# Performance work log

Measured on AMD Instinct MI355X. Metric: run time of the kernel, lower is better.

## Reference

```python
import jax, jax.numpy as jnp
import numpy as np

VOLRADIUS = 256.0  # init kwarg
NSTEPS = 64        # raymarch steps; dt chosen so NSTEPS*dt covers the box segment


def setup_inputs() -> dict:
    key = jax.random.key(0)
    ks = jax.random.split(key, 6)
    B, H, W, K, S = 1, 128, 128, 64, 16
    # camera ~2 box-radii in front of the volume (raw/world units, divided by VOLRADIUS in forward)
    viewpos = jnp.array([[0.0, 0.0, -2.0 * VOLRADIUS]], dtype=jnp.float32)
    viewpos = viewpos + 0.01 * VOLRADIUS * jax.random.normal(ks[0], (B, 3), dtype=jnp.float32)
    viewrot = jnp.tile(jnp.eye(3, dtype=jnp.float32)[None], (B, 1, 1))
    # pinhole rays looking at the box (tan(half-fov)=0.6 so the [-1,1]^3 box fills the frame)
    v, u = jnp.meshgrid(jnp.linspace(-1.0, 1.0, H), jnp.linspace(-1.0, 1.0, W), indexing='ij')
    d = jnp.stack([u * 0.6, v * 0.6, jnp.ones_like(u)], axis=-1)
    raydir = (d / jnp.linalg.norm(d, axis=-1, keepdims=True)).astype(jnp.float32)
    raydir = jnp.tile(raydir[None], (B, 1, 1, 1))
    # volumetric primitive payload + placement (normalized [-1,1] volume coords)
    template = jax.random.uniform(ks[1], (B, K, 4, S, S, S), dtype=jnp.float32)
    primpos = jax.random.uniform(ks[2], (B, K, 3), dtype=jnp.float32, minval=-0.7, maxval=0.7)
    q, _ = jnp.linalg.qr(jax.random.normal(ks[3], (B, K, 3, 3), dtype=jnp.float32))
    primrot = q.astype(jnp.float32)
    primscale = jax.random.uniform(ks[4], (B, K, 3), dtype=jnp.float32, minval=4.0, maxval=8.0)
    # raw dt (world units); forward divides by VOLRADIUS -> normalized step 2.2/NSTEPS
    dt = jnp.float32(2.2 / NSTEPS * VOLRADIUS)
    return dict(viewpos=viewpos, viewrot=viewrot, raydir=raydir, template=template,
                primpos=primpos, primrot=primrot, primscale=primscale, dt=dt)


def _sample_primitives(template, pos, primpos, primrot, primscale):
    """Sum of trilinearly-sampled RGBA over all primitives containing each point.
    template: [B,K,4,S,S,S], pos: [B,H,W,3] -> [B,H,W,4]"""
    B, K = template.shape[0], template.shape[1]
    S = template.shape[-1]
    xm = pos[:, :, :, None, :] - primpos[:, None, None, :, :]              # [B,H,W,K,3]
    # local coords: R^T (x - p) scaled by primscale (inverse half-extent)
    y = jnp.einsum('bhwki,bkij->bhwkj', xm, primrot) * primscale[:, None, None]
    inside = jnp.all(jnp.abs(y) < 1.0, axis=-1)                             # [B,H,W,K]
    g = (y + 1.0) * (0.5 * (S - 1))                                         # align_corners voxel coords
    g0 = jnp.clip(jnp.floor(g), 0.0, S - 2).astype(jnp.int32)
    f = g - g0.astype(g.dtype)
    x0, y0, z0 = g0[..., 0], g0[..., 1], g0[..., 2]                        # x->W, y->H, z->D
    fx, fy, fz = f[..., 0, None], f[..., 1, None], f[..., 2, None]
    tpl = jnp.moveaxis(template, 2, -1)                                     # [B,K,S,S,S,4]
    bidx = jnp.arange(B)[:, None, None, None]
    kidx = jnp.arange(K)[None, None, None, :]
    def gat(zi, yi, xi):
        return tpl[bidx, kidx, zi, yi, xi]                                  # [B,H,W,K,4]
    c00 = gat(z0, y0, x0) * (1 - fx) + gat(z0, y0, x0 + 1) * fx
    c01 = gat(z0, y0 + 1, x0) * (1 - fx) + gat(z0, y0 + 1, x0 + 1) * fx
    c10 = gat(z0 + 1, y0, x0) * (1 - fx) + gat(z0 + 1, y0, x0 + 1) * fx
    c11 = gat(z0 + 1, y0 + 1, x0) * (1 - fx) + gat(z0 + 1, y0 + 1, x0 + 1) * fx
    c = (c00 * (1 - fy) + c01 * fy) * (1 - fz) + (c10 * (1 - fy) + c11 * fy) * fz
    return jnp.einsum('bhwk,bhwkc->bhwc', inside.astype(c.dtype), c)        # [B,H,W,4]


def reference(viewpos, viewrot, raydir, template, primpos, primrot, primscale, dt):
    vp = viewpos / VOLRADIUS
    dtn = dt / VOLRADIUS
    # ray - AABB slab intersection with the [-1,1]^3 volume (no_grad in original)
    t1 = (-1.0 - vp[:, None, None, :]) / raydir
    t2 = (1.0 - vp[:, None, None, :]) / raydir
    tmin = jnp.maximum(jnp.minimum(t1[..., 0], t2[..., 0]),
                       jnp.maximum(jnp.minimum(t1[..., 1], t2[..., 1]),
                                   jnp.minimum(t1[..., 2], t2[..., 2])))
    tmax = jnp.minimum(jnp.maximum(t1[..., 0], t2[..., 0]),
                       jnp.minimum(jnp.maximum(t1[..., 1], t2[..., 1]),
                                   jnp.maximum(t1[..., 2], t2[..., 2])))
    inter = tmin < tmax
    tmin_ = jax.lax.stop_gradient(jnp.where(inter, tmin, 0.0))
    tmax_ = jax.lax.stop_gradient(jnp.where(inter, tmax, 0.0))
    t0 = jnp.maximum(tmin_, 0.0)
    rayposbeg = vp[:, None, None, :] + raydir * tmin_[..., None]
    rayposend = vp[:, None, None, :] + raydir * tmax_[..., None]

    def step(rgba, i):
        t = t0 + i.astype(t0.dtype) * dtn                                   # [B,H,W]
        valid = (t < tmax_).astype(rgba.dtype)
        pos = vp[:, None, None, :] + raydir * t[..., None]
        s = _sample_primitives(template, pos, primpos, primrot, primscale)  # [B,H,W,4]
        alpha = s[..., 3] * dtn * valid
        # saturating additive compositing (mvpraymarch): contrib = min(a+da,1)-a
        contrib = jnp.minimum(rgba[..., 3] + alpha, 1.0) - rgba[..., 3]
        rgba = rgba + jnp.concatenate([s[..., :3], jnp.ones_like(s[..., :1])], -1) * contrib[..., None]
        return rgba, None

    rgba0 = jnp.zeros(raydir.shape[:3] + (4,), raydir.dtype)
    rgba, _ = jax.lax.scan(step, rgba0, jnp.arange(NSTEPS))
    return (jnp.transpose(rgba, (0, 3, 1, 2)), rayposbeg, rayposend)
```

## Files before the change

### kernel.cpp

```cpp
#include <hip/hip_runtime.h>

#define HH 128
#define WW 128
#define KK 64
#define SS 16
#define S3 (SS * SS * SS)
#define VOLRADIUS 256.0f
#define CULL_EPS 1e-3f

template <int CTRL, int RM>
__device__ __forceinline__ float dpp_add(float x) {
    int y = __builtin_amdgcn_update_dpp(0, __float_as_int(x), CTRL, RM, 0xF, false);
    return x + __int_as_float(y);
}
__device__ __forceinline__ float wave_incl_scan(float x) {
    x = dpp_add<0x111, 0xF>(x);
    x = dpp_add<0x112, 0xF>(x);
    x = dpp_add<0x114, 0xF>(x);
    x = dpp_add<0x118, 0xF>(x);
    x = dpp_add<0x142, 0xA>(x);
    x = dpp_add<0x143, 0xC>(x);
    return x;
}

#define LERP4(a, b, f) make_float4(a.x*(1.f-(f)) + b.x*(f), a.y*(1.f-(f)) + b.y*(f), \
                                   a.z*(1.f-(f)) + b.z*(f), a.w*(1.f-(f)) + b.w*(f))

__global__ __launch_bounds__(256) void transpose_tpl(const float* __restrict__ tpl,
                                                     float4* __restrict__ tw) {
    int i = blockIdx.x * blockDim.x + threadIdx.x;
    if (i >= KK * S3) return;
    int k = i >> 12, v = i & (S3 - 1);
    const float* src = tpl + ((size_t)k * 4 * S3) + v;
    tw[i] = make_float4(src[0], src[S3], src[2 * S3], src[3 * S3]);
}

template <bool TR>
__global__ __launch_bounds__(256, 6) void raymarch_kernel(
    const float* __restrict__ viewpos,
    const float* __restrict__ raydir,
    const float* __restrict__ tpl,
    const float* __restrict__ primpos,
    const float* __restrict__ primrot,
    const float* __restrict__ primscale,
    const float* __restrict__ dtp,
    const float4* __restrict__ tw,
    float* __restrict__ out)
{
    const int lane = threadIdx.x & 63;
    const int pix  = (int)((blockIdx.x * blockDim.x + threadIdx.x) >> 6);
    if (pix >= HH * WW) return;

    const float vx = viewpos[0] / VOLRADIUS;
    const float vy = viewpos[1] / VOLRADIUS;
    const float vz = viewpos[2] / VOLRADIUS;
    const float dtn = dtp[0] / VOLRADIUS;

    const float Rx = raydir[pix*3+0], Ry = raydir[pix*3+1], Rz = raydir[pix*3+2];

    float t1x = (-1.f-vx)/Rx, t2x = (1.f-vx)/Rx;
    float t1y = (-1.f-vy)/Ry, t2y = (1.f-vy)/Ry;
    float t1z = (-1.f-vz)/Rz, t2z = (1.f-vz)/Rz;
    float tmin = fmaxf(fminf(t1x,t2x), fmaxf(fminf(t1y,t2y), fminf(t1z,t2z)));
    float tmax = fminf(fmaxf(t1x,t2x), fminf(fmaxf(t1y,t2y), fmaxf(t1z,t2z)));
    bool inter = tmin < tmax;
    float tmin_ = inter ? tmin : 0.f;
    float tmax_ = inter ? tmax : 0.f;
    float t0 = fmaxf(tmin_, 0.f);
    float t = t0 + (float)lane * dtn;
    const bool tvalid = t < tmax_;
    const float posx = vx + Rx*t;
    const float posy = vy + Ry*t;
    const float posz = vz + Rz*t;

    unsigned long long mask;
    {
        const float px = primpos[lane*3+0], py = primpos[lane*3+1], pz = primpos[lane*3+2];
        const float r00 = primrot[lane*9+0], r01 = primrot[lane*9+1], r02 = primrot[lane*9+2];
        const float r10 = primrot[lane*9+3], r11 = primrot[lane*9+4], r12 = primrot[lane*9+5];
        const float r20 = primrot[lane*9+6], r21 = primrot[lane*9+7], r22 = primrot[lane*9+8];
        const float sx = primscale[lane*3+0], sy = primscale[lane*3+1], sz = primscale[lane*3+2];
        float bb[3], dd[3];
        bb[0] = ((vx-px)*r00 + (vy-py)*r10 + (vz-pz)*r20) * sx;
        bb[1] = ((vx-px)*r01 + (vy-py)*r11 + (vz-pz)*r21) * sy;
        bb[2] = ((vx-px)*r02 + (vy-py)*r12 + (vz-pz)*r22) * sz;
        dd[0] = (Rx*r00 + Ry*r10 + Rz*r20) * sx;
        dd[1] = (Rx*r01 + Ry*r11 + Rz*r21) * sy;
        dd[2] = (Rx*r02 + Ry*r12 + Rz*r22) * sz;
        float tend = fminf(tmax_, t0 + 63.f*dtn);
        float te = t0, tx = tend;
#pragma unroll
        for (int j = 0; j < 3; ++j) {
            float ta, tb2;
            if (fabsf(dd[j]) > 1e-12f) {
                float inv = 1.f / dd[j];
                ta  = (-1.f - CULL_EPS - bb[j]) * inv;
                tb2 = ( 1.f + CULL_EPS - bb[j]) * inv;
            } else {
                bool ok = fabsf(bb[j]) <= 1.f + CULL_EPS;
                ta  = ok ? -3e38f :  3e38f;
                tb2 = ok ?  3e38f : -3e38f;
            }
            te = fmaxf(te, fminf(ta, tb2));
            tx = fminf(tx, fmaxf(ta, tb2));
        }
        mask = __ballot(te <= tx);
    }

    float sv0 = 0.f, sv1 = 0.f, sv2 = 0.f, sv3 = 0.f;

    while (mask) {
        const int ku = __builtin_amdgcn_readfirstlane(__ffsll(mask) - 1);
        mask &= mask - 1;
        const float qpx = primpos[ku*3+0], qpy = primpos[ku*3+1], qpz = primpos[ku*3+2];
        const float q00 = primrot[ku*9+0], q01 = primrot[ku*9+1], q02 = primrot[ku*9+2];
        const float q10 = primrot[ku*9+3], q11 = primrot[ku*9+4], q12 = primrot[ku*9+5];
        const float q20 = primrot[ku*9+6], q21 = primrot[ku*9+7], q22 = primrot[ku*9+8];
        const float qsx = primscale[ku*3+0], qsy = primscale[ku*3+1], qsz = primscale[ku*3+2];

        float xmx = posx-qpx, xmy = posy-qpy, xmz = posz-qpz;
        float y0 = (xmx*q00 + xmy*q10 + xmz*q20) * qsx;
        float y1 = (xmx*q01 + xmy*q11 + xmz*q21) * qsy;
        float y2 = (xmx*q02 + xmy*q12 + xmz*q22) * qsz;
        bool samp = tvalid && fabsf(y0) < 1.f && fabsf(y1) < 1.f && fabsf(y2) < 1.f;

        if (samp) {
            float gx = (y0+1.f)*(0.5f*(SS-1));
            float gy = (y1+1.f)*(0.5f*(SS-1));
            float gz = (y2+1.f)*(0.5f*(SS-1));
            int x0  = min(max((int)floorf(gx), 0), SS-2);
            int y0i = min(max((int)floorf(gy), 0), SS-2);
            int z0  = min(max((int)floorf(gz), 0), SS-2);
            float fx = gx-(float)x0, fy = gy-(float)y0i, fz = gz-(float)z0;
            int idx = z0*(SS*SS) + y0i*SS + x0;

            if (TR) {
                const float4* tb = tw + ((size_t)ku << 12) + idx;
                float4 c000 = tb[0],          c001 = tb[1];
                float4 c010 = tb[SS],         c011 = tb[SS+1];
                float4 c100 = tb[SS*SS],      c101 = tb[SS*SS+1];
                float4 c110 = tb[SS*SS+SS],   c111 = tb[SS*SS+SS+1];
                float4 c00 = LERP4(c000, c001, fx);
                float4 c01 = LERP4(c010, c011, fx);
                float4 c10 = LERP4(c100, c101, fx);
                float4 c11 = LERP4(c110, c111, fx);
                float4 e0  = LERP4(c00, c01, fy);
                float4 e1  = LERP4(c10, c11, fy);
                sv0 += e0.x*(1.f-fz) + e1.x*fz;
                sv1 += e0.y*(1.f-fz) + e1.y*fz;
                sv2 += e0.z*(1.f-fz) + e1.z*fz;
                sv3 += e0.w*(1.f-fz) + e1.w*fz;
            } else {
                const float* tp = tpl + (size_t)ku * (4 * S3);
                float sv[4];
#pragma unroll
                for (int c = 0; c < 4; ++c) {
                    const float* tc = tp + c * S3;
                    float c000 = tc[idx],              c001 = tc[idx+1];
                    float c010 = tc[idx+SS],           c011 = tc[idx+SS+1];
                    float c100 = tc[idx+SS*SS],        c101 = tc[idx+SS*SS+1];
                    float c110 = tc[idx+SS*SS+SS],     c111 = tc[idx+SS*SS+SS+1];
                    float c00 = c000*(1.f-fx) + c001*fx;
                    float c01 = c010*(1.f-fx) + c011*fx;
                    float c10 = c100*(1.f-fx) + c101*fx;
                    float c11 = c110*(1.f-fx) + c111*fx;
                    sv[c] = (c00*(1.f-fy) + c01*fy)*(1.f-fz)
                          + (c10*(1.f-fy) + c11*fy)*fz;
                }
                sv0 += sv[0]; sv1 += sv[1]; sv2 += sv[2]; sv3 += sv[3];
            }
        }
    }

    float alpha = tvalid ? sv3 * dtn : 0.f;
    float A = wave_incl_scan(alpha);
    float Aex = __shfl_up(A, 1, 64);
    if (lane == 0) Aex = 0.f;
    float contrib = fminf(Aex + alpha, 1.f) - fminf(Aex, 1.f);
    float cr = wave_incl_scan(sv0 * contrib);
    float cg = wave_incl_scan(sv1 * contrib);
    float cb = wave_incl_scan(sv2 * contrib);
    float At = fminf(A, 1.f);

    if (lane == 63) {
        out[0*HH*WW + pix] = cr;
        out[1*HH*WW + pix] = cg;
        out[2*HH*WW + pix] = cb;
        out[3*HH*WW + pix] = At;
        const int b1 = 4*HH*WW;
        out[b1 + pix*3+0] = vx + Rx*tmin_;
        out[b1 + pix*3+1] = vy + Ry*tmin_;
        out[b1 + pix*3+2] = vz + Rz*tmin_;
        const int b2 = b1 + HH*WW*3;
        out[b2 + pix*3+0] = vx + Rx*tmax_;
        out[b2 + pix*3+1] = vy + Ry*tmax_;
        out[b2 + pix*3+2] = vz + Rz*tmax_;
    }
}

extern "C" void kernel_launch(void* const* d_in, const int* in_sizes, int n_in,
                              void* d_out, int out_size, void* d_ws, size_t ws_size,
                              hipStream_t stream) {
    const float* viewpos   = (const float*)d_in[0];
    const float* raydir    = (const float*)d_in[2];
    const float* tpl       = (const float*)d_in[3];
    const float* primpos   = (const float*)d_in[4];
    const float* primrot   = (const float*)d_in[5];
    const float* primscale = (const float*)d_in[6];
    const float* dtp       = (const float*)d_in[7];
    float* out = (float*)d_out;

    const size_t twbytes = (size_t)KK * S3 * 4 * sizeof(float);
    dim3 block(256), grid(HH * WW * 64 / 256);

    if (ws_size >= twbytes) {
        transpose_tpl<<<dim3((KK * S3 + 255) / 256), block, 0, stream>>>(tpl, (float4*)d_ws);
        raymarch_kernel<true><<<grid, block, 0, stream>>>(
            viewpos, raydir, tpl, primpos, primrot, primscale, dtp,
            (const float4*)d_ws, out);
    } else {
        raymarch_kernel<false><<<grid, block, 0, stream>>>(
            viewpos, raydir, tpl, primpos, primrot, primscale, dtp,
            (const float4*)d_ws, out);
    }
}
```

Before: 36.06 us.

## Software-pipeline primitive gathers in two stages and remap wave-to-pixel order

The transposed-template path now issues the eight float4 gathers for the next culled primitive before interpolating the current one. This double-buffers loads across iterations to hide global memory latency. Out-of-box samples load index 0 with zero weight instead of branching. Launch bounds drop to 4 waves per EU to make room for the extra registers, and the wave-to-pixel mapping is permuted (pix = (wid&63)<<8 | wid>>6), which changes which rays share a block and how they hit the cache.

```diff
diff --git a/kernel.cpp b/kernel.cpp
--- a/kernel.cpp
+++ b/kernel.cpp
@@ -35,8 +35,55 @@
     tw[i] = make_float4(src[0], src[S3], src[2 * S3], src[3 * S3]);
 }
 
+#define DECL_STAGE(S) \
+    float4 c0##S, c1##S, c2##S, c3##S, c4##S, c5##S, c6##S, c7##S; \
+    float fx##S, fy##S, fz##S, w##S;
+
+#define STAGE_ISSUE(S) { \
+    const int ku = __builtin_amdgcn_readfirstlane(__ffsll(mask) - 1); \
+    mask &= mask - 1; \
+    const float qpx = primpos[ku*3+0], qpy = primpos[ku*3+1], qpz = primpos[ku*3+2]; \
+    const float q00 = primrot[ku*9+0], q01 = primrot[ku*9+1], q02 = primrot[ku*9+2]; \
+    const float q10 = primrot[ku*9+3], q11 = primrot[ku*9+4], q12 = primrot[ku*9+5]; \
+    const float q20 = primrot[ku*9+6], q21 = primrot[ku*9+7], q22 = primrot[ku*9+8]; \
+    const float qsx = primscale[ku*3+0], qsy = primscale[ku*3+1], qsz = primscale[ku*3+2]; \
+    float xmx = posx-qpx, xmy = posy-qpy, xmz = posz-qpz; \
+    float y0 = (xmx*q00 + xmy*q10 + xmz*q20) * qsx; \
+    float y1 = (xmx*q01 + xmy*q11 + xmz*q21) * qsy; \
+    float y2 = (xmx*q02 + xmy*q12 + xmz*q22) * qsz; \
+    bool samp = tvalid && fabsf(y0) < 1.f && fabsf(y1) < 1.f && fabsf(y2) < 1.f; \
+    float gx = (y0+1.f)*(0.5f*(SS-1)); \
+    float gy = (y1+1.f)*(0.5f*(SS-1)); \
+    float gz = (y2+1.f)*(0.5f*(SS-1)); \
+    int x0  = min(max((int)floorf(gx), 0), SS-2); \
+    int y0i = min(max((int)floorf(gy), 0), SS-2); \
+    int z0  = min(max((int)floorf(gz), 0), SS-2); \
+    fx##S = gx-(float)x0; fy##S = gy-(float)y0i; fz##S = gz-(float)z0; \
+    w##S  = samp ? 1.f : 0.f; \
+    int idx = samp ? (z0*(SS*SS) + y0i*SS + x0) : 0; \
+    const float4* tb = tw + ((size_t)ku << 12) + idx; \
+    c0##S = tb[0];          c1##S = tb[1]; \
+    c2##S = tb[SS];         c3##S = tb[SS+1]; \
+    c4##S = tb[SS*SS];      c5##S = tb[SS*SS+1]; \
+    c6##S = tb[SS*SS+SS];   c7##S = tb[SS*SS+SS+1]; \
+}
+
+#define STAGE_CONSUME(S) { \
+    float4 c00 = LERP4(c0##S, c1##S, fx##S); \
+    float4 c01 = LERP4(c2##S, c3##S, fx##S); \
+    float4 c10 = LERP4(c4##S, c5##S, fx##S); \
+    float4 c11 = LERP4(c6##S, c7##S, fx##S); \
+    float4 e0  = LERP4(c00, c01, fy##S); \
+    float4 e1  = LERP4(c10, c11, fy##S); \
+    float fzv = fz##S, wv = w##S; \
+    sv0 += (e0.x*(1.f-fzv) + e1.x*fzv) * wv; \
+    sv1 += (e0.y*(1.f-fzv) + e1.y*fzv) * wv; \
+    sv2 += (e0.z*(1.f-fzv) + e1.z*fzv) * wv; \
+    sv3 += (e0.w*(1.f-fzv) + e1.w*fzv) * wv; \
+}
+
 template <bool TR>
-__global__ __launch_bounds__(256, 6) void raymarch_kernel(
+__global__ __launch_bounds__(256, 4) void raymarch_kernel(
     const float* __restrict__ viewpos,
     const float* __restrict__ raydir,
     const float* __restrict__ tpl,
@@ -48,8 +95,9 @@
     float* __restrict__ out)
 {
     const int lane = threadIdx.x & 63;
-    const int pix  = (int)((blockIdx.x * blockDim.x + threadIdx.x) >> 6);
-    if (pix >= HH * WW) return;
+    const int wid  = (int)((blockIdx.x * blockDim.x + threadIdx.x) >> 6);
+    if (wid >= HH * WW) return;
+    const int pix = ((wid & 63) << 8) | (wid >> 6);
 
     const float vx = viewpos[0] / VOLRADIUS;
     const float vy = viewpos[1] / VOLRADIUS;
@@ -109,48 +157,45 @@
 
     float sv0 = 0.f, sv1 = 0.f, sv2 = 0.f, sv3 = 0.f;
 
-    while (mask) {
-        const int ku = __builtin_amdgcn_readfirstlane(__ffsll(mask) - 1);
-        mask &= mask - 1;
-        const float qpx = primpos[ku*3+0], qpy = primpos[ku*3+1], qpz = primpos[ku*3+2];
-        const float q00 = primrot[ku*9+0], q01 = primrot[ku*9+1], q02 = primrot[ku*9+2];
-        const float q10 = primrot[ku*9+3], q11 = primrot[ku*9+4], q12 = primrot[ku*9+5];
-        const float q20 = primrot[ku*9+6], q21 = primrot[ku*9+7], q22 = primrot[ku*9+8];
-        const float qsx = primscale[ku*3+0], qsy = primscale[ku*3+1], qsz = primscale[ku*3+2];
-
-        float xmx = posx-qpx, xmy = posy-qpy, xmz = posz-qpz;
-        float y0 = (xmx*q00 + xmy*q10 + xmz*q20) * qsx;
-        float y1 = (xmx*q01 + xmy*q11 + xmz*q21) * qsy;
-        float y2 = (xmx*q02 + xmy*q12 + xmz*q22) * qsz;
-        bool samp = tvalid && fabsf(y0) < 1.f && fabsf(y1) < 1.f && fabsf(y2) < 1.f;
-
-        if (samp) {
-            float gx = (y0+1.f)*(0.5f*(SS-1));
-            float gy = (y1+1.f)*(0.5f*(SS-1));
-            float gz = (y2+1.f)*(0.5f*(SS-1));
-            int x0  = min(max((int)floorf(gx), 0), SS-2);
-            int y0i = min(max((int)floorf(gy), 0), SS-2);
-            int z0  = min(max((int)floorf(gz), 0), SS-2);
-            float fx = gx-(float)x0, fy = gy-(float)y0i, fz = gz-(float)z0;
-            int idx = z0*(SS*SS) + y0i*SS + x0;
-
-            if (TR) {
-                const float4* tb = tw + ((size_t)ku << 12) + idx;
-                float4 c000 = tb[0],          c001 = tb[1];
-                float4 c010 = tb[SS],         c011 = tb[SS+1];
-                float4 c100 = tb[SS*SS],      c101 = tb[SS*SS+1];
-                float4 c110 = tb[SS*SS+SS],   c111 = tb[SS*SS+SS+1];
-                float4 c00 = LERP4(c000, c001, fx);
-                float4 c01 = LERP4(c010, c011, fx);
-                float4 c10 = LERP4(c100, c101, fx);
-                float4 c11 = LERP4(c110, c111, fx);
-                float4 e0  = LERP4(c00, c01, fy);
-                float4 e1  = LERP4(c10, c11, fy);
-                sv0 += e0.x*(1.f-fz) + e1.x*fz;
-                sv1 += e0.y*(1.f-fz) + e1.y*fz;
-                sv2 += e0.z*(1.f-fz) + e1.z*fz;
-                sv3 += e0.w*(1.f-fz) + e1.w*fz;
-            } else {
+    if (TR) {
+        DECL_STAGE(A)
+        DECL_STAGE(B)
+        if (mask) {
+            STAGE_ISSUE(A)
+            for (;;) {
+                bool haveB = (mask != 0ull);
+                if (haveB) STAGE_ISSUE(B)
+                STAGE_CONSUME(A)
+                if (!haveB) break;
+                bool haveA = (mask != 0ull);
+                if (haveA) STAGE_ISSUE(A)
+                STAGE_CONSUME(B)
+                if (!haveA) break;
+            }
+        }
+    } else {
+        while (mask) {
+            const int ku = __builtin_amdgcn_readfirstlane(__ffsll(mask) - 1);
+            mask &= mask - 1;
+            const float qpx = primpos[ku*3+0], qpy = primpos[ku*3+1], qpz = primpos[ku*3+2];
+            const float q00 = primrot[ku*9+0], q01 = primrot[ku*9+1], q02 = primrot[ku*9+2];
+            const float q10 = primrot[ku*9+3], q11 = primrot[ku*9+4], q12 = primrot[ku*9+5];
+            const float q20 = primrot[ku*9+6], q21 = primrot[ku*9+7], q22 = primrot[ku*9+8];
+            const float qsx = primscale[ku*3+0], qsy = primscale[ku*3+1], qsz = primscale[ku*3+2];
+            float xmx = posx-qpx, xmy = posy-qpy, xmz = posz-qpz;
+            float y0 = (xmx*q00 + xmy*q10 + xmz*q20) * qsx;
+            float y1 = (xmx*q01 + xmy*q11 + xmz*q21) * qsy;
+            float y2 = (xmx*q02 + xmy*q12 + xmz*q22) * qsz;
+            bool samp = tvalid && fabsf(y0) < 1.f && fabsf(y1) < 1.f && fabsf(y2) < 1.f;
+            if (samp) {
+                float gx = (y0+1.f)*(0.5f*(SS-1));
+                float gy = (y1+1.f)*(0.5f*(SS-1));
+                float gz = (y2+1.f)*(0.5f*(SS-1));
+                int x0  = min(max((int)floorf(gx), 0), SS-2);
+                int y0i = min(max((int)floorf(gy), 0), SS-2);
+                int z0  = min(max((int)floorf(gz), 0), SS-2);
+                float fx = gx-(float)x0, fy = gy-(float)y0i, fz = gz-(float)z0;
+                int idx = z0*(SS*SS) + y0i*SS + x0;
                 const float* tp = tpl + (size_t)ku * (4 * S3);
                 float sv[4];
 #pragma unroll
```

Measured after the change: 38.11 us. 1.06x slower.

## Compact primitive-step work pairs across lanes with LDS atomic accumulation

Applied to the files above, without the earlier changes.

Rather than each lane owning one march step and looping over every candidate primitive, each primitive lane now computes the range of steps its culled box covers. A wave prefix-scan of these counts yields a compacted list of (primitive, step) pairs, processed 64 at a time, with binary search over shuffled start offsets to find each lane's primitive. Results go into per-wave LDS accumulators through atomics. Pixel ordering is also remapped across waves, and the occupancy hint drops from 6 to 4, trading extra shuffles, atomics and LDS for less lane divergence on empty samples.

```diff
diff --git a/kernel.cpp b/kernel.cpp
--- a/kernel.cpp
+++ b/kernel.cpp
@@ -9,17 +9,27 @@
 #define CULL_EPS 1e-3f
 
 template <int CTRL, int RM>
-__device__ __forceinline__ float dpp_add(float x) {
+__device__ __forceinline__ float dpp_addf(float x) {
     int y = __builtin_amdgcn_update_dpp(0, __float_as_int(x), CTRL, RM, 0xF, false);
     return x + __int_as_float(y);
 }
 __device__ __forceinline__ float wave_incl_scan(float x) {
-    x = dpp_add<0x111, 0xF>(x);
-    x = dpp_add<0x112, 0xF>(x);
-    x = dpp_add<0x114, 0xF>(x);
-    x = dpp_add<0x118, 0xF>(x);
-    x = dpp_add<0x142, 0xA>(x);
-    x = dpp_add<0x143, 0xC>(x);
+    x = dpp_addf<0x111, 0xF>(x);
+    x = dpp_addf<0x112, 0xF>(x);
+    x = dpp_addf<0x114, 0xF>(x);
+    x = dpp_addf<0x118, 0xF>(x);
+    x = dpp_addf<0x142, 0xA>(x);
+    x = dpp_addf<0x143, 0xC>(x);
+    return x;
+}
+__device__ __forceinline__ int wave_incl_scan_addi(int x) {
+    int y;
+    y = __builtin_amdgcn_update_dpp(0, x, 0x111, 0xF, 0xF, false); x += y;
+    y = __builtin_amdgcn_update_dpp(0, x, 0x112, 0xF, 0xF, false); x += y;
+    y = __builtin_amdgcn_update_dpp(0, x, 0x114, 0xF, 0xF, false); x += y;
+    y = __builtin_amdgcn_update_dpp(0, x, 0x118, 0xF, 0xF, false); x += y;
+    y = __builtin_amdgcn_update_dpp(0, x, 0x142, 0xA, 0xF, false); x += y;
+    y = __builtin_amdgcn_update_dpp(0, x, 0x143, 0xC, 0xF, false); x += y;
     return x;
 }
 
@@ -36,7 +46,7 @@
 }
 
 template <bool TR>
-__global__ __launch_bounds__(256, 6) void raymarch_kernel(
+__global__ __launch_bounds__(256, 4) void raymarch_kernel(
     const float* __restrict__ viewpos,
     const float* __restrict__ raydir,
     const float* __restrict__ tpl,
@@ -47,9 +57,15 @@
     const float4* __restrict__ tw,
     float* __restrict__ out)
 {
-    const int lane = threadIdx.x & 63;
-    const int pix  = (int)((blockIdx.x * blockDim.x + threadIdx.x) >> 6);
-    if (pix >= HH * WW) return;
+    const int lane = (int)(threadIdx.x & 63);
+    const int wvid = (int)(threadIdx.x >> 6);
+    const int wid = __builtin_amdgcn_readfirstlane(
+        (int)((blockIdx.x * blockDim.x + threadIdx.x) >> 6));
+    if (wid >= HH * WW) return;
+    const int pix = ((wid & 63) << 8) | (wid >> 6);
+
+    __shared__ float4 accs[4][64];
+    accs[wvid][lane] = make_float4(0.f, 0.f, 0.f, 0.f);
 
     const float vx = viewpos[0] / VOLRADIUS;
     const float vy = viewpos[1] / VOLRADIUS;
@@ -67,19 +83,15 @@
     float tmin_ = inter ? tmin : 0.f;
     float tmax_ = inter ? tmax : 0.f;
     float t0 = fmaxf(tmin_, 0.f);
-    float t = t0 + (float)lane * dtn;
-    const bool tvalid = t < tmax_;
-    const float posx = vx + Rx*t;
-    const float posy = vy + Ry*t;
-    const float posz = vz + Rz*t;
-
-    unsigned long long mask;
+
+    const float px = primpos[lane*3+0], py = primpos[lane*3+1], pz = primpos[lane*3+2];
+    const float r00 = primrot[lane*9+0], r01 = primrot[lane*9+1], r02 = primrot[lane*9+2];
+    const float r10 = primrot[lane*9+3], r11 = primrot[lane*9+4], r12 = primrot[lane*9+5];
+    const float r20 = primrot[lane*9+6], r21 = primrot[lane*9+7], r22 = primrot[lane*9+8];
+    const float sx = primscale[lane*3+0], sy = primscale[lane*3+1], sz = primscale[lane*3+2];
+
+    int ilo = 0, icnt = 0;
     {
-        const float px = primpos[lane*3+0], py = primpos[lane*3+1], pz = primpos[lane*3+2];
-        const float r00 = primrot[lane*9+0], r01 = primrot[lane*9+1], r02 = primrot[lane*9+2];
-        const float r10 = primrot[lane*9+3], r11 = primrot[lane*9+4], r12 = primrot[lane*9+5];
-        const float r20 = primrot[lane*9+6], r21 = primrot[lane*9+7], r22 = primrot[lane*9+8];
-        const float sx = primscale[lane*3+0], sy = primscale[lane*3+1], sz = primscale[lane*3+2];
         float bb[3], dd[3];
         bb[0] = ((vx-px)*r00 + (vy-py)*r10 + (vz-pz)*r20) * sx;
         bb[1] = ((vx-px)*r01 + (vy-py)*r11 + (vz-pz)*r21) * sy;
@@ -104,38 +116,62 @@
             te = fmaxf(te, fminf(ta, tb2));
             tx = fminf(tx, fmaxf(ta, tb2));
         }
-        mask = __ballot(te <= tx);
-    }
-
-    float sv0 = 0.f, sv1 = 0.f, sv2 = 0.f, sv3 = 0.f;
-
-    while (mask) {
-        const int ku = __builtin_amdgcn_readfirstlane(__ffsll(mask) - 1);
-        mask &= mask - 1;
-        const float qpx = primpos[ku*3+0], qpy = primpos[ku*3+1], qpz = primpos[ku*3+2];
-        const float q00 = primrot[ku*9+0], q01 = primrot[ku*9+1], q02 = primrot[ku*9+2];
-        const float q10 = primrot[ku*9+3], q11 = primrot[ku*9+4], q12 = primrot[ku*9+5];
-        const float q20 = primrot[ku*9+6], q21 = primrot[ku*9+7], q22 = primrot[ku*9+8];
-        const float qsx = primscale[ku*3+0], qsy = primscale[ku*3+1], qsz = primscale[ku*3+2];
-
-        float xmx = posx-qpx, xmy = posy-qpy, xmz = posz-qpz;
-        float y0 = (xmx*q00 + xmy*q10 + xmz*q20) * qsx;
-        float y1 = (xmx*q01 + xmy*q11 + xmz*q21) * qsy;
-        float y2 = (xmx*q02 + xmy*q12 + xmz*q22) * qsz;
-        bool samp = tvalid && fabsf(y0) < 1.f && fabsf(y1) < 1.f && fabsf(y2) < 1.f;
-
-        if (samp) {
-            float gx = (y0+1.f)*(0.5f*(SS-1));
-            float gy = (y1+1.f)*(0.5f*(SS-1));
-            float gz = (y2+1.f)*(0.5f*(SS-1));
-            int x0  = min(max((int)floorf(gx), 0), SS-2);
-            int y0i = min(max((int)floorf(gy), 0), SS-2);
-            int z0  = min(max((int)floorf(gz), 0), SS-2);
-            float fx = gx-(float)x0, fy = gy-(float)y0i, fz = gz-(float)z0;
-            int idx = z0*(SS*SS) + y0i*SS + x0;
-
-            if (TR) {
-                const float4* tb = tw + ((size_t)ku << 12) + idx;
+        if (te <= tx) {
+            ilo = max(0, (int)floorf((te - t0) / dtn));
+            int ihi = min(63, (int)ceilf((tx - t0) / dtn));
+            icnt = max(0, ihi - ilo + 1);
+        }
+    }
+
+    float sv0, sv1, sv2, sv3;
+
+    if (TR) {
+        const int Ainc  = wave_incl_scan_addi(icnt);
+        const int start = Ainc - icnt;
+        const int Ctot  = __builtin_amdgcn_readlane(Ainc, 63);
+        const int nw    = (Ctot + 63) >> 6;
+
+        for (int b = 0; b < nw; ++b) {
+            const int s  = (b << 6) + lane;
+            const bool act = s < Ctot;
+
+            int p = 0;
+#pragma unroll
+            for (int st = 32; st > 0; st >>= 1) {
+                int cand = p | st;
+                int sp = __shfl(start, cand, 64);
+                if (sp <= s) p = cand;
+            }
+            const int pst = __shfl(start, p, 64);
+            const int il  = __shfl(ilo,   p, 64);
+            const int ic  = __shfl(icnt,  p, 64);
+            const int i   = il + (s - pst);
+            const bool inrange = act && (s - pst) < ic;
+
+            float qpx = __shfl(px, p, 64), qpy = __shfl(py, p, 64), qpz = __shfl(pz, p, 64);
+            float q00 = __shfl(r00, p, 64), q01 = __shfl(r01, p, 64), q02 = __shfl(r02, p, 64);
+            float q10 = __shfl(r10, p, 64), q11 = __shfl(r11, p, 64), q12 = __shfl(r12, p, 64);
+            float q20 = __shfl(r20, p, 64), q21 = __shfl(r21, p, 64), q22 = __shfl(r22, p, 64);
+            float qsx = __shfl(sx, p, 64), qsy = __shfl(sy, p, 64), qsz = __shfl(sz, p, 64);
+
+            float ti = t0 + (float)i * dtn;
+            float posx = vx + Rx*ti, posy = vy + Ry*ti, posz = vz + Rz*ti;
+            float xmx = posx-qpx, xmy = posy-qpy, xmz = posz-qpz;
+            float y0 = (xmx*q00 + xmy*q10 + xmz*q20) * qsx;
+            float y1 = (xmx*q01 + xmy*q11 + xmz*q21) * qsy;
+            float y2 = (xmx*q02 + xmy*q12 + xmz*q22) * qsz;
+            bool samp = inrange && (ti < tmax_) &&
+                        fabsf(y0) < 1.f && fabsf(y1) < 1.f && fabsf(y2) < 1.f;
+            if (samp) {
+                float gx = (y0+1.f)*(0.5f*(SS-1));
+                float gy = (y1+1.f)*(0.5f*(SS-1));
+                float gz = (y2+1.f)*(0.5f*(SS-1));
+                int x0  = min(max((int)floorf(gx), 0), SS-2);
+                int y0i = min(max((int)floorf(gy), 0), SS-2);
+                int z0  = min(max((int)floorf(gz), 0), SS-2);
+                float fx = gx-(float)x0, fy = gy-(float)y0i, fz = gz-(float)z0;
+                int idx = z0*(SS*SS) + y0i*SS + x0;
+                const float4* tb = tw + ((size_t)p << 12) + idx;
                 float4 c000 = tb[0],          c001 = tb[1];
                 float4 c010 = tb[SS],         c011 = tb[SS+1];
                 float4 c100 = tb[SS*SS],      c101 = tb[SS*SS+1];
@@ -146,11 +182,43 @@
                 float4 c11 = LERP4(c110, c111, fx);
                 float4 e0  = LERP4(c00, c01, fy);
                 float4 e1  = LERP4(c10, c11, fy);
-                sv0 += e0.x*(1.f-fz) + e1.x*fz;
-                sv1 += e0.y*(1.f-fz) + e1.y*fz;
-                sv2 += e0.z*(1.f-fz) + e1.z*fz;
-                sv3 += e0.w*(1.f-fz) + e1.w*fz;
-            } else {
+                float* ap = (float*)&accs[wvid][i];
+                atomicAdd(ap + 0, e0.x*(1.f-fz) + e1.x*fz);
+                atomicAdd(ap + 1, e0.y*(1.f-fz) + e1.y*fz);
+                atomicAdd(ap + 2, e0.z*(1.f-fz) + e1.z*fz);
+                atomicAdd(ap + 3, e0.w*(1.f-fz) + e1.w*fz);
+            }
+        }
+        float4 a = accs[wvid][lane];
+        sv0 = a.x; sv1 = a.y; sv2 = a.z; sv3 = a.w;
+    } else {
+        unsigned long long mask = __ballot(icnt > 0);
+        const float t = t0 + (float)lane * dtn;
+        const bool tvalid = t < tmax_;
+        const float posx = vx + Rx*t, posy = vy + Ry*t, posz = vz + Rz*t;
+        sv0 = sv1 = sv2 = sv3 = 0.f;
+        while (mask) {
+            const int ku = __builtin_amdgcn_readfirstlane(__ffsll(mask) - 1);
+            mask &= mask - 1;
+            const float qpx = primpos[ku*3+0], qpy = primpos[ku*3+1], qpz = primpos[ku*3+2];
+            const float q00 = primrot[ku*9+0], q01 = primrot[ku*9+1], q02 = primrot[ku*9+2];
+            const float q10 = primrot[ku*9+3], q11 = primrot[ku*9+4], q12 = primrot[ku*9+5];
+            const float q20 = primrot[ku*9+6], q21 = primrot[ku*9+7], q22 = primrot[ku*9+8];
+            const float qsx = primscale[ku*3+0], qsy = primscale[ku*3+1], qsz = primscale[ku*3+2];
+            float xmx = posx-qpx, xmy = posy-qpy, xmz = posz-qpz;
+            float y0 = (xmx*q00 + xmy*q10 + xmz*q20) * qsx;
+            float y1 = (xmx*q01 + xmy*q11 + xmz*q21) * qsy;
+            float y2 = (xmx*q02 + xmy*q12 + xmz*q22) * qsz;
+            bool samp = tvalid && fabsf(y0) < 1.f && fabsf(y1) < 1.f && fabsf(y2) < 1.f;
+            if (samp) {
+                float gx = (y0+1.f)*(0.5f*(SS-1));
+                float gy = (y1+1.f)*(0.5f*(SS-1));
+                float gz = (y2+1.f)*(0.5f*(SS-1));
+                int x0  = min(max((int)floorf(gx), 0), SS-2);
+                int y0i = min(max((int)floorf(gy), 0), SS-2);
+                int z0  = min(max((int)floorf(gz), 0), SS-2);
+                float fx = gx-(float)x0, fy = gy-(float)y0i, fz = gz-(float)z0;
+                int idx = z0*(SS*SS) + y0i*SS + x0;
                 const float* tp = tpl + (size_t)ku * (4 * S3);
                 float sv[4];
 #pragma unroll
@@ -172,6 +240,8 @@
         }
     }
 
+    const float tl = t0 + (float)lane * dtn;
+    const bool tvalid = tl < tmax_;
     float alpha = tvalid ? sv3 * dtn : 0.f;
     float A = wave_incl_scan(alpha);
     float Aex = __shfl_up(A, 1, 64);
```

Result: faster. 30.93 us (-14.2%).
